# Performance work log

Measured on AMD Instinct MI355X. Metric: run time of the kernel, lower is better.

Reference implementation:

```python
import jax, jax.numpy as jnp
import numpy as np

B, S, E = 4, 4096, 128  # batch, seq_len, embedding_dim (quaternion groups)
D = 4 * E               # flattened feature dim fed to the Linear layers


def setup_inputs() -> dict:
    key = jax.random.key(0)
    ks = jax.random.split(key, 9)
    scale_w = 1.0 / np.sqrt(D).astype(np.float32)
    return {
        "query": jax.random.normal(ks[0], (B, S, E, 4), dtype=jnp.float32),
        "key": jax.random.normal(ks[1], (B, S, E, 4), dtype=jnp.float32),
        "value": jax.random.normal(ks[2], (B, S, E, 4), dtype=jnp.float32),
        "Wq": jax.random.normal(ks[3], (D, D), dtype=jnp.float32) * scale_w,
        "bq": jax.random.normal(ks[4], (D,), dtype=jnp.float32) * 0.01,
        "Wk": jax.random.normal(ks[5], (D, D), dtype=jnp.float32) * scale_w,
        "bk": jax.random.normal(ks[6], (D,), dtype=jnp.float32) * 0.01,
        "Wv": jax.random.normal(ks[7], (D, D), dtype=jnp.float32) * scale_w,
        "bv": jax.random.normal(ks[8], (D,), dtype=jnp.float32) * 0.01,
    }


def reference(query, key, value, Wq, bq, Wk, bk, Wv, bv):
    b, s = query.shape[0], query.shape[1]
    e = query.shape[2]  # embedding_dim
    # flatten quaternion dim: [B,S,E,4] -> [B,S,4E]
    q = query.reshape(b, s, -1)
    k = key.reshape(b, key.shape[1], -1)
    v = value.reshape(b, value.shape[1], -1)
    # torch nn.Linear: x @ W^T + bias
    Q = (q @ Wq.T + bq).reshape(b, s, -1, 4)
    K = (k @ Wk.T + bk).reshape(b, key.shape[1], -1, 4)
    V = (v @ Wv.T + bv).reshape(b, value.shape[1], -1, 4)
    # full QK^T over quaternion-grouped dims: [B,S,S]
    scores = jnp.einsum('bseq,bkeq->bsk', Q, K) / jnp.sqrt(jnp.float32(e))
    weights = jax.nn.softmax(scores, axis=-1)
    # faithful to the source: weights are summed over k and scale V at position s
    output = jnp.einsum('bsk,bseq->bseq', weights, V)
    return output, weights
```

## Files before the change

kernel.cpp:

```cpp
#include <hip/hip_runtime.h>
#include <cstdint>

typedef _Float16 h1;
typedef _Float16 h4 __attribute__((ext_vector_type(4)));
typedef _Float16 h8 __attribute__((ext_vector_type(8)));
typedef float    f4 __attribute__((ext_vector_type(4)));
typedef float    f32x4 __attribute__((ext_vector_type(4)));

#define NB 4
#define SL 4096
#define DD 512
#define MM (NB*SL)
#define SHIFT 12.0f

__global__ __launch_bounds__(256) void convert_all(
    const float* __restrict__ Xq, const float* __restrict__ Xk, const float* __restrict__ Xv,
    const float* __restrict__ Wq, const float* __restrict__ Wk, const float* __restrict__ Wv,
    h1* __restrict__ Xh, h1* __restrict__ Wh)
{
    const int xper = MM*DD/4;
    const int wper = DD*DD/4;
    const int xtot = 3*xper;
    int i = blockIdx.x * 256 + threadIdx.x;
    const float* src;
    h1* dst;
    int j;
    if (i < xtot) {
        int mat = i / xper; j = i - mat*xper;
        src = (mat==0) ? Xq : (mat==1 ? Xk : Xv);
        dst = Xh + (size_t)mat*MM*DD;
    } else {
        int t = i - xtot;
        if (t >= 3*wper) return;
        int mat = t / wper; j = t - mat*wper;
        src = (mat==0) ? Wq : (mat==1 ? Wk : Wv);
        dst = Wh + (size_t)mat*DD*DD;
    }
    f4 v = ((const f4*)src)[j];
    h4 hv;
    hv[0]=(h1)v[0]; hv[1]=(h1)v[1]; hv[2]=(h1)v[2]; hv[3]=(h1)v[3];
    ((h4*)dst)[j] = hv;
}

__device__ __forceinline__ void stage_tile(const h1* __restrict__ gbase,
                                           h1* lds, int w, int l)
{
    #pragma unroll
    for (int j = 0; j < 4; j++) {
        const int cc  = w*4 + j;
        const int row = cc*8 + (l >> 3);
        const int sc  = (l & 7) ^ (l >> 3);
        const h1* src = gbase + (size_t)row * DD + sc*8;
        void* dst = (char*)lds + cc*1024;
        __builtin_amdgcn_global_load_lds(
            (const __attribute__((address_space(1))) uint32_t*)src,
            (__attribute__((address_space(3))) uint32_t*)dst, 16, 0, 0);
    }
}

__device__ __forceinline__ h8 lds_frag(const h1* lds, int row, int lc)
{
    const int chunk = lc ^ (row & 7);
    return *(const h8*)(lds + row*64 + chunk*8);
}

__global__ __launch_bounds__(256) void proj_gemm(
    const h1* __restrict__ Xh, const h1* __restrict__ Wh,
    const float* __restrict__ bq, const float* __restrict__ bk, const float* __restrict__ bv,
    h1* __restrict__ Qh, h1* __restrict__ Kh, float* __restrict__ Vout)
{
    const int prj = blockIdx.z;
    const h1* __restrict__ X    = Xh + (size_t)prj * MM * DD;
    const h1* __restrict__ W    = Wh + (size_t)prj * DD * DD;
    const float* __restrict__ bias = (prj==0) ? bq : (prj==1 ? bk : bv);

    const int m0 = blockIdx.y * 128;
    const int n0 = blockIdx.x * 128;

    __shared__ h1 As[128*64];
    __shared__ h1 Bs[128*64];

    const int tid  = threadIdx.x;
    const int lane = tid & 63;
    const int wid  = tid >> 6;
    const int wm = wid >> 1, wn = wid & 1;
    const int g  = lane >> 4, c = lane & 15;

    f32x4 acc[4][4];
    #pragma unroll
    for (int i = 0; i < 4; i++)
        #pragma unroll
        for (int j = 0; j < 4; j++) acc[i][j] = (f32x4){0.f, 0.f, 0.f, 0.f};

    for (int k0 = 0; k0 < DD; k0 += 64) {
        __syncthreads();
        stage_tile(X + (size_t)m0 * DD + k0, As, wid, lane);
        stage_tile(W + (size_t)n0 * DD + k0, Bs, wid, lane);
        __syncthreads();
        #pragma unroll
        for (int kk = 0; kk < 2; kk++) {
            h8 af[4], bf[4];
            #pragma unroll
            for (int mf = 0; mf < 4; mf++) af[mf] = lds_frag(As, wm*64 + mf*16 + c, kk*4 + g);
            #pragma unroll
            for (int nf = 0; nf < 4; nf++) bf[nf] = lds_frag(Bs, wn*64 + nf*16 + c, kk*4 + g);
            #pragma unroll
            for (int mf = 0; mf < 4; mf++)
                #pragma unroll
                for (int nf = 0; nf < 4; nf++)
                    acc[mf][nf] = __builtin_amdgcn_mfma_f32_16x16x32_f16(af[mf], bf[nf], acc[mf][nf], 0, 0, 0);
        }
    }

    float bv4[4];
    #pragma unroll
    for (int nf = 0; nf < 4; nf++) bv4[nf] = bias[n0 + wn*64 + nf*16 + c];

    #pragma unroll
    for (int mf = 0; mf < 4; mf++) {
        #pragma unroll
        for (int i = 0; i < 4; i++) {
            const int row = m0 + wm*64 + mf*16 + g*4 + i;
            #pragma unroll
            for (int nf = 0; nf < 4; nf++) {
                const int col = n0 + wn*64 + nf*16 + c;
                float vv = acc[mf][nf][i] + bv4[nf];
                if (prj == 0)      Qh[(size_t)row*DD + col] = (h1)vv;
                else if (prj == 1) Kh[(size_t)row*DD + col] = (h1)vv;
                else               Vout[(size_t)row*DD + col] = vv;
            }
        }
    }
}

__device__ __forceinline__ void stage_slot32(const h1* __restrict__ gbase,
                                             char* ldsbase, int w, int l)
{
    #pragma unroll
    for (int j = 0; j < 2; j++) {
        const int lc  = j*512 + w*64 + l;
        const int row = lc >> 2;
        const int ch  = lc & 3;
        const int sc  = ch ^ ((row >> 1) & 3);
        const h1* src = gbase + (size_t)row * DD + sc*8;
        __builtin_amdgcn_global_load_lds(
            (const __attribute__((address_space(1))) uint32_t*)src,
            (__attribute__((address_space(3))) uint32_t*)(ldsbase + (size_t)(j*512 + w*64)*16),
            16, 0, 0);
    }
}

__device__ __forceinline__ h8 frag32(const h1* lds, int row, int g)
{
    const int ch = g ^ ((row >> 1) & 3);
    return *(const h8*)(lds + row*32 + ch*8);
}

__global__ __launch_bounds__(512) void scores_gemm_8ph(
    const h1* __restrict__ Qh, const h1* __restrict__ Kh,
    h1* __restrict__ Eh,
    float* __restrict__ partial)
{
    const int orig = blockIdx.x;
    const int swz  = (orig & 7) * 128 + (orig >> 3);
    const int b  = swz >> 8;
    const int t_ = swz & 255;
    const int ty = t_ >> 4;
    const int tx = t_ & 15;
    const int m0 = ty * 256;
    const int n0 = tx * 256;
    const h1* __restrict__ Qb = Qh + (size_t)b * SL * DD;
    const h1* __restrict__ Kb = Kh + (size_t)b * SL * DD;

    __shared__ h1 Albuf[4*256*32];
    __shared__ h1 Blbuf[4*256*32];
    const int SLOT_H = 256*32;
    const int SLOT_B = SLOT_H*2;

    const int tid  = threadIdx.x;
    const int lane = tid & 63;
    const int wid  = tid >> 6;
    const int wm = wid >> 2;
    const int wn = wid & 3;
    const int g  = lane >> 4, c = lane & 15;

    f32x4 acc[8][4];
    #pragma unroll
    for (int i = 0; i < 8; i++)
        #pragma unroll
        for (int j = 0; j < 4; j++) acc[i][j] = (f32x4){0.f, 0.f, 0.f, 0.f};

    #pragma unroll
    for (int kt = 0; kt < 3; ++kt) {
        stage_slot32(Qb + (size_t)m0*DD + kt*32, (char*)Albuf + kt*SLOT_B, wid, lane);
        stage_slot32(Kb + (size_t)n0*DD + kt*32, (char*)Blbuf + kt*SLOT_B, wid, lane);
    }
    asm volatile("s_waitcnt vmcnt(8)" ::: "memory");
    __builtin_amdgcn_s_barrier();

    for (int kt = 0; kt < 16; ++kt) {
        const int cur = kt & 3;
        const h1* Abase = Albuf + cur*SLOT_H;
        const h1* Bbase = Blbuf + cur*SLOT_H;

        h8 af[4], bf[4];
        #pragma unroll
        for (int fm = 0; fm < 4; fm++) af[fm] = frag32(Abase, wm*128 + fm*16 + c, g);
        #pragma unroll
        for (int fn = 0; fn < 4; fn++) bf[fn] = frag32(Bbase, wn*64 + fn*16 + c, g);

        if (kt <= 12) {
            const int nk = kt + 3, ns = nk & 3;
            stage_slot32(Qb + (size_t)m0*DD + nk*32, (char*)Albuf + ns*SLOT_B, wid, lane);
            stage_slot32(Kb + (size_t)n0*DD + nk*32, (char*)Blbuf + ns*SLOT_B, wid, lane);
        }

        __builtin_amdgcn_s_barrier();
        asm volatile("s_waitcnt lgkmcnt(0)" ::: "memory");
        __builtin_amdgcn_sched_barrier(0);
        __builtin_amdgcn_s_setprio(1);
        #pragma unroll
        for (int fm = 0; fm < 4; fm++)
            #pragma unroll
            for (int fn = 0; fn < 4; fn++)
                acc[fm][fn] = __builtin_amdgcn_mfma_f32_16x16x32_f16(af[fm], bf[fn], acc[fm][fn], 0, 0, 0);
        __builtin_amdgcn_s_setprio(0);
        __builtin_amdgcn_s_barrier();

        #pragma unroll
        for (int fm = 0; fm < 4; fm++) af[fm] = frag32(Abase, wm*128 + 64 + fm*16 + c, g);

        __builtin_amdgcn_s_barrier();
        asm volatile("s_waitcnt lgkmcnt(0)" ::: "memory");
        __builtin_amdgcn_sched_barrier(0);
        __builtin_amdgcn_s_setprio(1);
        #pragma unroll
        for (int fm = 0; fm < 4; fm++)
            #pragma unroll
            for (int fn = 0; fn < 4; fn++)
                acc[4+fm][fn] = __builtin_amdgcn_mfma_f32_16x16x32_f16(af[fm], bf[fn], acc[4+fm][fn], 0, 0, 0);
        __builtin_amdgcn_s_setprio(0);

        if (kt <= 12)      { asm volatile("s_waitcnt vmcnt(8)" ::: "memory"); }
        else if (kt == 13) { asm volatile("s_waitcnt vmcnt(4)" ::: "memory"); }
        else if (kt == 14) { asm volatile("s_waitcnt vmcnt(0)" ::: "memory"); }
        __builtin_amdgcn_s_barrier();
    }

    const float inv_scale = 0.08838834764831845f;
    #pragma unroll
    for (int mf = 0; mf < 8; mf++) {
        #pragma unroll
        for (int i = 0; i < 4; i++) {
            const int row = m0 + wm*128 + mf*16 + g*4 + i;
            h1* erow = Eh + ((size_t)b * SL + row) * SL;
            float rsum = 0.f;
            #pragma unroll
            for (int nf = 0; nf < 4; nf++) {
                const int col = n0 + wn*64 + nf*16 + c;
                float e = __expf(fmaf(acc[mf][nf][i], inv_scale, -SHIFT));
                erow[col] = (h1)e;
                rsum += e;
            }
            #pragma unroll
            for (int off = 1; off < 16; off <<= 1) rsum += __shfl_xor(rsum, off);
            if (c == 0)
                partial[((size_t)b * SL + row) * 64 + tx * 4 + wn] = rsum;
        }
    }
}

__global__ __launch_bounds__(256) void rowsum_inv(
    const float* __restrict__ partial, float* __restrict__ invrow)
{
    int row = blockIdx.x * 256 + threadIdx.x;
    const f4* p = (const f4*)(partial + (size_t)row * 64);
    float s = 0.f;
    #pragma unroll
    for (int i = 0; i < 16; i++) { f4 v = p[i]; s += v[0] + v[1] + v[2] + v[3]; }
    invrow[row] = 1.0f / s;
}

__global__ __launch_bounds__(256) void normalize_k(
    const h1* __restrict__ Eh, const float* __restrict__ invrow,
    float* __restrict__ Wout)
{
    const size_t total8 = (size_t)NB * SL * SL / 8;
    size_t i = (size_t)blockIdx.x * blockDim.x + threadIdx.x;
    const size_t stride = (size_t)gridDim.x * blockDim.x;
    for (; i < total8; i += stride) {
        const int row = (int)(i >> 9);
        h8 v = ((const h8*)Eh)[i];
        const float s = invrow[row];
        f4 o0, o1;
        #pragma unroll
        for (int j = 0; j < 4; j++) { o0[j] = (float)v[j] * s; o1[j] = (float)v[4+j] * s; }
        ((f4*)Wout)[i*2]   = o0;
        ((f4*)Wout)[i*2+1] = o1;
    }
}

extern "C" void kernel_launch(void* const* d_in, const int* in_sizes, int n_in,
                              void* d_out, int out_size, void* d_ws, size_t ws_size,
                              hipStream_t stream)
{
    const float* q  = (const float*)d_in[0];
    const float* k  = (const float*)d_in[1];
    const float* v  = (const float*)d_in[2];
    const float* Wq = (const float*)d_in[3];
    const float* bq = (const float*)d_in[4];
    const float* Wk = (const float*)d_in[5];
    const float* bk = (const float*)d_in[6];
    const float* Wv = (const float*)d_in[7];
    const float* bv = (const float*)d_in[8];

    float* out  = (float*)d_out;
    float* Vout = out;
    float* Wout = out + (size_t)MM * DD;

    char* ws = (char*)d_ws;
    h1* Xh = (h1*)ws;
    h1* Wh = (h1*)(ws + (size_t)3*MM*DD*2);
    h1* Qh = (h1*)((char*)Wh + (size_t)3*DD*DD*2);
    h1* Kh = (h1*)((char*)Qh + (size_t)MM*DD*2);
    float* partial = (float*)((char*)Kh + (size_t)MM*DD*2);
    float* invrow  = (float*)((char*)partial + (size_t)MM*64*4);
    h1* Eh = (h1*)((char*)invrow + (size_t)MM*4);

    const int conv_chunks = (3*MM*DD + 3*DD*DD) / 4;
    convert_all<<<(conv_chunks + 255)/256, 256, 0, stream>>>(q, k, v, Wq, Wk, Wv, Xh, Wh);
    proj_gemm<<<dim3(4, 128, 3), 256, 0, stream>>>(Xh, Wh, bq, bk, bv, Qh, Kh, Vout);
    scores_gemm_8ph<<<1024, 512, 0, stream>>>(Qh, Kh, Eh, partial);
    rowsum_inv<<<MM / 256, 256, 0, stream>>>(partial, invrow);
    normalize_k<<<2048, 256, 0, stream>>>(Eh, invrow, Wout);
}
```

Before: 285.3 us.

## Fuse all stages into one persistent cooperative kernel with grid syncs

Replaces the five separate launches (convert, projection GEMM, scores GEMM, row-sum inverse, normalize) with a single cooperative kernel of 256 blocks of 512 threads. Stages are separated by grid.sync, and blocks loop over tiles: the projection uses narrower 128x128 tiles split across 8 waves, and each block computes four 256x256 score tiles in turn. The aim is to remove launch gaps and inter-kernel tails. In exchange, occupancy is capped at one large block per CU, there are four grid-wide barriers, and the projection tiling is changed.

```diff
diff --git a/kernel.cpp b/kernel.cpp
--- a/kernel.cpp
+++ b/kernel.cpp
@@ -1,5 +1,8 @@
 #include <hip/hip_runtime.h>
+#include <hip/hip_cooperative_groups.h>
 #include <cstdint>
+
+namespace cg = cooperative_groups;
 
 typedef _Float16 h1;
 typedef _Float16 h4 __attribute__((ext_vector_type(4)));
@@ -12,49 +15,26 @@
 #define DD 512
 #define MM (NB*SL)
 #define SHIFT 12.0f
-
-__global__ __launch_bounds__(256) void convert_all(
-    const float* __restrict__ Xq, const float* __restrict__ Xk, const float* __restrict__ Xv,
-    const float* __restrict__ Wq, const float* __restrict__ Wk, const float* __restrict__ Wv,
-    h1* __restrict__ Xh, h1* __restrict__ Wh)
-{
-    const int xper = MM*DD/4;
-    const int wper = DD*DD/4;
-    const int xtot = 3*xper;
-    int i = blockIdx.x * 256 + threadIdx.x;
-    const float* src;
-    h1* dst;
-    int j;
-    if (i < xtot) {
-        int mat = i / xper; j = i - mat*xper;
-        src = (mat==0) ? Xq : (mat==1 ? Xk : Xv);
-        dst = Xh + (size_t)mat*MM*DD;
-    } else {
-        int t = i - xtot;
-        if (t >= 3*wper) return;
-        int mat = t / wper; j = t - mat*wper;
-        src = (mat==0) ? Wq : (mat==1 ? Wk : Wv);
-        dst = Wh + (size_t)mat*DD*DD;
-    }
-    f4 v = ((const f4*)src)[j];
-    h4 hv;
-    hv[0]=(h1)v[0]; hv[1]=(h1)v[1]; hv[2]=(h1)v[2]; hv[3]=(h1)v[3];
-    ((h4*)dst)[j] = hv;
-}
-
-__device__ __forceinline__ void stage_tile(const h1* __restrict__ gbase,
-                                           h1* lds, int w, int l)
+#define NTHREADS 131072
+
+struct Params {
+    const float *Xq, *Xk, *Xv, *Wq, *Wk, *Wv, *bq, *bk, *bv;
+    h1 *Xh, *Wh, *Qh, *Kh, *Eh;
+    float *partial, *invrow, *Vout, *Wout;
+};
+
+__device__ __forceinline__ void stage_half(const h1* __restrict__ gbase,
+                                           char* ldsbase, int w, int l)
 {
     #pragma unroll
-    for (int j = 0; j < 4; j++) {
-        const int cc  = w*4 + j;
+    for (int j = 0; j < 2; j++) {
+        const int cc  = w*2 + j;
         const int row = cc*8 + (l >> 3);
         const int sc  = (l & 7) ^ (l >> 3);
         const h1* src = gbase + (size_t)row * DD + sc*8;
-        void* dst = (char*)lds + cc*1024;
         __builtin_amdgcn_global_load_lds(
             (const __attribute__((address_space(1))) uint32_t*)src,
-            (__attribute__((address_space(3))) uint32_t*)dst, 16, 0, 0);
+            (__attribute__((address_space(3))) uint32_t*)(ldsbase + cc*1024), 16, 0, 0);
     }
 }
 
@@ -62,75 +42,6 @@
 {
     const int chunk = lc ^ (row & 7);
     return *(const h8*)(lds + row*64 + chunk*8);
-}
-
-__global__ __launch_bounds__(256) void proj_gemm(
-    const h1* __restrict__ Xh, const h1* __restrict__ Wh,
-    const float* __restrict__ bq, const float* __restrict__ bk, const float* __restrict__ bv,
-    h1* __restrict__ Qh, h1* __restrict__ Kh, float* __restrict__ Vout)
-{
-    const int prj = blockIdx.z;
-    const h1* __restrict__ X    = Xh + (size_t)prj * MM * DD;
-    const h1* __restrict__ W    = Wh + (size_t)prj * DD * DD;
-    const float* __restrict__ bias = (prj==0) ? bq : (prj==1 ? bk : bv);
-
-    const int m0 = blockIdx.y * 128;
-    const int n0 = blockIdx.x * 128;
-
-    __shared__ h1 As[128*64];
-    __shared__ h1 Bs[128*64];
-
-    const int tid  = threadIdx.x;
-    const int lane = tid & 63;
-    const int wid  = tid >> 6;
-    const int wm = wid >> 1, wn = wid & 1;
-    const int g  = lane >> 4, c = lane & 15;
-
-    f32x4 acc[4][4];
-    #pragma unroll
-    for (int i = 0; i < 4; i++)
-        #pragma unroll
-        for (int j = 0; j < 4; j++) acc[i][j] = (f32x4){0.f, 0.f, 0.f, 0.f};
-
-    for (int k0 = 0; k0 < DD; k0 += 64) {
-        __syncthreads();
-        stage_tile(X + (size_t)m0 * DD + k0, As, wid, lane);
-        stage_tile(W + (size_t)n0 * DD + k0, Bs, wid, lane);
-        __syncthreads();
-        #pragma unroll
-        for (int kk = 0; kk < 2; kk++) {
-            h8 af[4], bf[4];
-            #pragma unroll
-            for (int mf = 0; mf < 4; mf++) af[mf] = lds_frag(As, wm*64 + mf*16 + c, kk*4 + g);
-            #pragma unroll
-            for (int nf = 0; nf < 4; nf++) bf[nf] = lds_frag(Bs, wn*64 + nf*16 + c, kk*4 + g);
-            #pragma unroll
-            for (int mf = 0; mf < 4; mf++)
-                #pragma unroll
-                for (int nf = 0; nf < 4; nf++)
-                    acc[mf][nf] = __builtin_amdgcn_mfma_f32_16x16x32_f16(af[mf], bf[nf], acc[mf][nf], 0, 0, 0);
-        }
-    }
-
-    float bv4[4];
-    #pragma unroll
-    for (int nf = 0; nf < 4; nf++) bv4[nf] = bias[n0 + wn*64 + nf*16 + c];
-
-    #pragma unroll
-    for (int mf = 0; mf < 4; mf++) {
-        #pragma unroll
-        for (int i = 0; i < 4; i++) {
-            const int row = m0 + wm*64 + mf*16 + g*4 + i;
-            #pragma unroll
-            for (int nf = 0; nf < 4; nf++) {
-                const int col = n0 + wn*64 + nf*16 + c;
-                float vv = acc[mf][nf][i] + bv4[nf];
-                if (prj == 0)      Qh[(size_t)row*DD + col] = (h1)vv;
-                else if (prj == 1) Kh[(size_t)row*DD + col] = (h1)vv;
-                else               Vout[(size_t)row*DD + col] = vv;
-            }
-        }
-    }
 }
 
 __device__ __forceinline__ void stage_slot32(const h1* __restrict__ gbase,
@@ -156,147 +67,239 @@
     return *(const h8*)(lds + row*32 + ch*8);
 }
 
-__global__ __launch_bounds__(512) void scores_gemm_8ph(
-    const h1* __restrict__ Qh, const h1* __restrict__ Kh,
-    h1* __restrict__ Eh,
-    float* __restrict__ partial)
-{
-    const int orig = blockIdx.x;
-    const int swz  = (orig & 7) * 128 + (orig >> 3);
-    const int b  = swz >> 8;
-    const int t_ = swz & 255;
-    const int ty = t_ >> 4;
-    const int tx = t_ & 15;
-    const int m0 = ty * 256;
-    const int n0 = tx * 256;
-    const h1* __restrict__ Qb = Qh + (size_t)b * SL * DD;
-    const h1* __restrict__ Kb = Kh + (size_t)b * SL * DD;
-
-    __shared__ h1 Albuf[4*256*32];
-    __shared__ h1 Blbuf[4*256*32];
-    const int SLOT_H = 256*32;
-    const int SLOT_B = SLOT_H*2;
+__global__ __launch_bounds__(512) void mega(Params p)
+{
+    cg::grid_group grid = cg::this_grid();
+    __shared__ char smem[131072];
 
     const int tid  = threadIdx.x;
+    const int bid  = blockIdx.x;
+    const int gtid = bid * 512 + tid;
     const int lane = tid & 63;
     const int wid  = tid >> 6;
-    const int wm = wid >> 2;
-    const int wn = wid & 3;
-    const int g  = lane >> 4, c = lane & 15;
-
-    f32x4 acc[8][4];
-    #pragma unroll
-    for (int i = 0; i < 8; i++)
+    const int g    = lane >> 4, c = lane & 15;
+
+    {
+        const int xper = MM*DD/4;
+        const int wper = DD*DD/4;
+        const int xtot = 3*xper;
+        const int tot  = xtot + 3*wper;
+        for (int i = gtid; i < tot; i += NTHREADS) {
+            const float* src;
+            h1* dst;
+            int j;
+            if (i < xtot) {
+                int mat = i / xper; j = i - mat*xper;
+                src = (mat==0) ? p.Xq : (mat==1 ? p.Xk : p.Xv);
+                dst = p.Xh + (size_t)mat*MM*DD;
+            } else {
+                int t = i - xtot;
+                int mat = t / wper; j = t - mat*wper;
+                src = (mat==0) ? p.Wq : (mat==1 ? p.Wk : p.Wv);
+                dst = p.Wh + (size_t)mat*DD*DD;
+            }
+            f4 v = ((const f4*)src)[j];
+            h4 hv;
+            hv[0]=(h1)v[0]; hv[1]=(h1)v[1]; hv[2]=(h1)v[2]; hv[3]=(h1)v[3];
+            ((h4*)dst)[j] = hv;
+        }
+    }
+    grid.sync();
+
+    {
+        h1* As = (h1*)smem;
+        h1* Bs = (h1*)(smem + 16384);
+        const int wm = wid >> 2;
+        const int wn = wid & 3;
+
+        for (int tile = bid; tile < 1536; tile += 256) {
+            const int prj = tile >> 9;
+            const int rem = tile & 511;
+            const int m0  = (rem >> 2) * 128;
+            const int n0  = (rem & 3) * 128;
+            const h1* X = p.Xh + (size_t)prj * MM * DD;
+            const h1* W = p.Wh + (size_t)prj * DD * DD;
+            const float* bias = (prj==0) ? p.bq : (prj==1 ? p.bk : p.bv);
+
+            f32x4 acc[4][2];
+            #pragma unroll
+            for (int i = 0; i < 4; i++)
+                #pragma unroll
+                for (int j = 0; j < 2; j++) acc[i][j] = (f32x4){0.f,0.f,0.f,0.f};
+
+            for (int k0 = 0; k0 < DD; k0 += 64) {
+                __syncthreads();
+                stage_half(X + (size_t)m0 * DD + k0, (char*)As, wid, lane);
+                stage_half(W + (size_t)n0 * DD + k0, (char*)Bs, wid, lane);
+                __syncthreads();
+                #pragma unroll
+                for (int kk = 0; kk < 2; kk++) {
+                    h8 af[4], bf[2];
+                    #pragma unroll
+                    for (int mf = 0; mf < 4; mf++) af[mf] = lds_frag(As, wm*64 + mf*16 + c, kk*4 + g);
+                    #pragma unroll
+                    for (int nf = 0; nf < 2; nf++) bf[nf] = lds_frag(Bs, wn*32 + nf*16 + c, kk*4 + g);
+                    #pragma unroll
+                    for (int mf = 0; mf < 4; mf++)
+                        #pragma unroll
+                        for (int nf = 0; nf < 2; nf++)
+                            acc[mf][nf] = __builtin_amdgcn_mfma_f32_16x16x32_f16(af[mf], bf[nf], acc[mf][nf], 0, 0, 0);
+                }
+            }
+
+            float bv2[2];
+            #pragma unroll
+            for (int nf = 0; nf < 2; nf++) bv2[nf] = bias[n0 + wn*32 + nf*16 + c];
+
+            #pragma unroll
+            for (int mf = 0; mf < 4; mf++) {
+                #pragma unroll
+                for (int i = 0; i < 4; i++) {
+                    const int row = m0 + wm*64 + mf*16 + g*4 + i;
+                    #pragma unroll
+                    for (int nf = 0; nf < 2; nf++) {
+                        const int col = n0 + wn*32 + nf*16 + c;
+                        float vv = acc[mf][nf][i] + bv2[nf];
+                        if (prj == 0)      p.Qh[(size_t)row*DD + col] = (h1)vv;
+                        else if (prj == 1) p.Kh[(size_t)row*DD + col] = (h1)vv;
+                        else               p.Vout[(size_t)row*DD + col] = vv;
+                    }
+                }
+            }
+            __syncthreads();
+        }
+    }
+    grid.sync();
+
+    {
+        h1* Albuf = (h1*)smem;
+        h1* Blbuf = (h1*)(smem + 65536);
+        const int SLOT_H = 256*32;
+        const int SLOT_B = SLOT_H*2;
+        const int wm = wid >> 2;
+        const int wn = wid & 3;
+        const float inv_scale = 0.08838834764831845f;
+
+        #pragma unroll 1
+        for (int tt = 0; tt < 4; tt++) {
+            const int t_ = bid*4 + tt;
+            const int b  = t_ >> 8;
+            const int ty = (t_ >> 4) & 15;
+            const int tx = t_ & 15;
+            const int m0 = ty * 256;
+            const int n0 = tx * 256;
+            const h1* __restrict__ Qb = p.Qh + (size_t)b * SL * DD;
+            const h1* __restrict__ Kb = p.Kh + (size_t)b * SL * DD;
+
+            f32x4 acc[8][4];
+            #pragma unroll
+            for (int i = 0; i < 8; i++)
+                #pragma unroll
+                for (int j = 0; j < 4; j++) acc[i][j] = (f32x4){0.f,0.f,0.f,0.f};
+
+            __syncthreads();
+            #pragma unroll
+            for (int kt = 0; kt < 3; ++kt) {
+                stage_slot32(Qb + (size_t)m0*DD + kt*32, (char*)Albuf + kt*SLOT_B, wid, lane);
+                stage_slot32(Kb + (size_t)n0*DD + kt*32, (char*)Blbuf + kt*SLOT_B, wid, lane);
+            }
+            asm volatile("s_waitcnt vmcnt(8)" ::: "memory");
+            __builtin_amdgcn_s_barrier();
+
+            for (int kt = 0; kt < 16; ++kt) {
+                const int cur = kt & 3;
+                const h1* Abase = Albuf + cur*SLOT_H;
+                const h1* Bbase = Blbuf + cur*SLOT_H;
+
+                h8 af[4], bf[4];
+                #pragma unroll
+                for (int fm = 0; fm < 4; fm++) af[fm] = frag32(Abase, wm*128 + fm*16 + c, g);
+                #pragma unroll
+                for (int fn = 0; fn < 4; fn++) bf[fn] = frag32(Bbase, wn*64 + fn*16 + c, g);
+
+                if (kt <= 12) {
+                    const int nk = kt + 3, ns = nk & 3;
+                    stage_slot32(Qb + (size_t)m0*DD + nk*32, (char*)Albuf + ns*SLOT_B, wid, lane);
+                    stage_slot32(Kb + (size_t)n0*DD + nk*32, (char*)Blbuf + ns*SLOT_B, wid, lane);
+                }
+
+                __builtin_amdgcn_s_barrier();
+                asm volatile("s_waitcnt lgkmcnt(0)" ::: "memory");
+                __builtin_amdgcn_sched_barrier(0);
+                __builtin_amdgcn_s_setprio(1);
+                #pragma unroll
+                for (int fm = 0; fm < 4; fm++)
+                    #pragma unroll
+                    for (int fn = 0; fn < 4; fn++)
+                        acc[fm][fn] = __builtin_amdgcn_mfma_f32_16x16x32_f16(af[fm], bf[fn], acc[fm][fn], 0, 0, 0);
+                __builtin_amdgcn_s_setprio(0);
+                __builtin_amdgcn_s_barrier();
+
+                #pragma unroll
+                for (int fm = 0; fm < 4; fm++) af[fm] = frag32(Abase, wm*128 + 64 + fm*16 + c, g);
+
+                __builtin_amdgcn_s_barrier();
+                asm volatile("s_waitcnt lgkmcnt(0)" ::: "memory");
+                __builtin_amdgcn_sched_barrier(0);
+                __builtin_amdgcn_s_setprio(1);
+                #pragma unroll
+                for (int fm = 0; fm < 4; fm++)
+                    #pragma unroll
+                    for (int fn = 0; fn < 4; fn++)
+                        acc[4+fm][fn] = __builtin_amdgcn_mfma_f32_16x16x32_f16(af[fm], bf[fn], acc[4+fm][fn], 0, 0, 0);
+                __builtin_amdgcn_s_setprio(0);
+
+                if (kt <= 12)      { asm volatile("s_waitcnt vmcnt(8)" ::: "memory"); }
+                else if (kt == 13) { asm volatile("s_waitcnt vmcnt(4)" ::: "memory"); }
+                else if (kt == 14) { asm volatile("s_waitcnt vmcnt(0)" ::: "memory"); }
+                __builtin_amdgcn_s_barrier();
+            }
+
+            #pragma unroll
+            for (int mf = 0; mf < 8; mf++) {
+                #pragma unroll
+                for (int i = 0; i < 4; i++) {
+                    const int row = m0 + wm*128 + mf*16 + g*4 + i;
+                    h1* erow = p.Eh + ((size_t)b * SL + row) * SL;
+                    float rsum = 0.f;
+                    #pragma unroll
+                    for (int nf = 0; nf < 4; nf++) {
+                        const int col = n0 + wn*64 + nf*16 + c;
+                        float e = __expf(fmaf(acc[mf][nf][i], inv_scale, -SHIFT));
+                        erow[col] = (h1)e;
+                        rsum += e;
+                    }
+                    #pragma unroll
+                    for (int off = 1; off < 16; off <<= 1) rsum += __shfl_xor(rsum, off);
+                    if (c == 0)
+                        p.partial[((size_t)b * SL + row) * 64 + tx * 4 + wn] = rsum;
+                }
+            }
+        }
+    }
+    grid.sync();
+
+    if (gtid < MM) {
+        const f4* pp = (const f4*)(p.partial + (size_t)gtid * 64);
+        float s = 0.f;
         #pragma unroll
-        for (int j = 0; j < 4; j++) acc[i][j] = (f32x4){0.f, 0.f, 0.f, 0.f};
-
-    #pragma unroll
-    for (int kt = 0; kt < 3; ++kt) {
-        stage_slot32(Qb + (size_t)m0*DD + kt*32, (char*)Albuf + kt*SLOT_B, wid, lane);
-        stage_slot32(Kb + (size_t)n0*DD + kt*32, (char*)Blbuf + kt*SLOT_B, wid, lane);
-    }
-    asm volatile("s_waitcnt vmcnt(8)" ::: "memory");
-    __builtin_amdgcn_s_barrier();
-
-    for (int kt = 0; kt < 16; ++kt) {
-        const int cur = kt & 3;
-        const h1* Abase = Albuf + cur*SLOT_H;
-        const h1* Bbase = Blbuf + cur*SLOT_H;
-
-        h8 af[4], bf[4];
-        #pragma unroll
-        for (int fm = 0; fm < 4; fm++) af[fm] = frag32(Abase, wm*128 + fm*16 + c, g);
-        #pragma unroll
-        for (int fn = 0; fn < 4; fn++) bf[fn] = frag32(Bbase, wn*64 + fn*16 + c, g);
-
-        if (kt <= 12) {
-            const int nk = kt + 3, ns = nk & 3;
-            stage_slot32(Qb + (size_t)m0*DD + nk*32, (char*)Albuf + ns*SLOT_B, wid, lane);
-            stage_slot32(Kb + (size_t)n0*DD + nk*32, (char*)Blbuf + ns*SLOT_B, wid, lane);
+        for (int i = 0; i < 16; i++) { f4 v = pp[i]; s += v[0] + v[1] + v[2] + v[3]; }
+        p.invrow[gtid] = 1.0f / s;
+    }
+    grid.sync();
+
+    {
+        const size_t total8 = (size_t)NB * SL * SL / 8;
+        for (size_t i = gtid; i < total8; i += NTHREADS) {
+            const int row = (int)(i >> 9);
+            h8 v = ((const h8*)p.Eh)[i];
+            const float s = p.invrow[row];
+            f4 o0, o1;
+            #pragma unroll
+            for (int j = 0; j < 4; j++) { o0[j] = (float)v[j] * s; o1[j] = (float)v[4+j] * s; }
+            ((f4*)p.Wout)[i*2]   = o0;
+            ((f4*)p.Wout)[i*2+1] = o1;
         }
-
-        __builtin_amdgcn_s_barrier();
-        asm volatile("s_waitcnt lgkmcnt(0)" ::: "memory");
-        __builtin_amdgcn_sched_barrier(0);
-        __builtin_amdgcn_s_setprio(1);
-        #pragma unroll
-        for (int fm = 0; fm < 4; fm++)
-            #pragma unroll
-            for (int fn = 0; fn < 4; fn++)
-                acc[fm][fn] = __builtin_amdgcn_mfma_f32_16x16x32_f16(af[fm], bf[fn], acc[fm][fn], 0, 0, 0);
-        __builtin_amdgcn_s_setprio(0);
-        __builtin_amdgcn_s_barrier();
-
-        #pragma unroll
-        for (int fm = 0; fm < 4; fm++) af[fm] = frag32(Abase, wm*128 + 64 + fm*16 + c, g);
-
-        __builtin_amdgcn_s_barrier();
-        asm volatile("s_waitcnt lgkmcnt(0)" ::: "memory");
-        __builtin_amdgcn_sched_barrier(0);
-        __builtin_amdgcn_s_setprio(1);
-        #pragma unroll
-        for (int fm = 0; fm < 4; fm++)
-            #pragma unroll
-            for (int fn = 0; fn < 4; fn++)
-                acc[4+fm][fn] = __builtin_amdgcn_mfma_f32_16x16x32_f16(af[fm], bf[fn], acc[4+fm][fn], 0, 0, 0);
-        __builtin_amdgcn_s_setprio(0);
-
-        if (kt <= 12)      { asm volatile("s_waitcnt vmcnt(8)" ::: "memory"); }
-        else if (kt == 13) { asm volatile("s_waitcnt vmcnt(4)" ::: "memory"); }
-        else if (kt == 14) { asm volatile("s_waitcnt vmcnt(0)" ::: "memory"); }
-        __builtin_amdgcn_s_barrier();
-    }
-
-    const float inv_scale = 0.08838834764831845f;
-    #pragma unroll
-    for (int mf = 0; mf < 8; mf++) {
-        #pragma unroll
-        for (int i = 0; i < 4; i++) {
-            const int row = m0 + wm*128 + mf*16 + g*4 + i;
-            h1* erow = Eh + ((size_t)b * SL + row) * SL;
-            float rsum = 0.f;
-            #pragma unroll
-            for (int nf = 0; nf < 4; nf++) {
-                const int col = n0 + wn*64 + nf*16 + c;
-                float e = __expf(fmaf(acc[mf][nf][i], inv_scale, -SHIFT));
-                erow[col] = (h1)e;
-                rsum += e;
-            }
-            #pragma unroll
-            for (int off = 1; off < 16; off <<= 1) rsum += __shfl_xor(rsum, off);
-            if (c == 0)
-                partial[((size_t)b * SL + row) * 64 + tx * 4 + wn] = rsum;
-        }
-    }
-}
-
-__global__ __launch_bounds__(256) void rowsum_inv(
-    const float* __restrict__ partial, float* __restrict__ invrow)
-{
-    int row = blockIdx.x * 256 + threadIdx.x;
-    const f4* p = (const f4*)(partial + (size_t)row * 64);
-    float s = 0.f;
-    #pragma unroll
-    for (int i = 0; i < 16; i++) { f4 v = p[i]; s += v[0] + v[1] + v[2] + v[3]; }
-    invrow[row] = 1.0f / s;
-}
-
-__global__ __launch_bounds__(256) void normalize_k(
-    const h1* __restrict__ Eh, const float* __restrict__ invrow,
-    float* __restrict__ Wout)
-{
-    const size_t total8 = (size_t)NB * SL * SL / 8;
-    size_t i = (size_t)blockIdx.x * blockDim.x + threadIdx.x;
-    const size_t stride = (size_t)gridDim.x * blockDim.x;
-    for (; i < total8; i += stride) {
-        const int row = (int)(i >> 9);
-        h8 v = ((const h8*)Eh)[i];
-        const float s = invrow[row];
-        f4 o0, o1;
-        #pragma unroll
-        for (int j = 0; j < 4; j++) { o0[j] = (float)v[j] * s; o1[j] = (float)v[4+j] * s; }
-        ((f4*)Wout)[i*2]   = o0;
-        ((f4*)Wout)[i*2+1] = o1;
     }
 }
 
@@ -304,33 +307,31 @@
                               void* d_out, int out_size, void* d_ws, size_t ws_size,
                               hipStream_t stream)
 {
-    const float* q  = (const float*)d_in[0];
-    const float* k  = (const float*)d_in[1];
-    const float* v  = (const float*)d_in[2];
-    const float* Wq = (const float*)d_in[3];
-    const float* bq = (const float*)d_in[4];
-    const float* Wk = (const float*)d_in[5];
-    const float* bk = (const float*)d_in[6];
-    const float* Wv = (const float*)d_in[7];
-    const float* bv = (const float*)d_in[8];
-
     float* out  = (float*)d_out;
-    float* Vout = out;
-    float* Wout = out + (size_t)MM * DD;
-
     char* ws = (char*)d_ws;
-    h1* Xh = (h1*)ws;
-    h1* Wh = (h1*)(ws + (size_t)3*MM*DD*2);
-    h1* Qh = (h1*)((char*)Wh + (size_t)3*DD*DD*2);
-    h1* Kh = (h1*)((char*)Qh + (size_t)MM*DD*2);
-    float* partial = (float*)((char*)Kh + (size_t)MM*DD*2);
-    float* invrow  = (float*)((char*)partial + (size_t)MM*64*4);
-    h1* Eh = (h1*)((char*)invrow + (size_t)MM*4);
-
-    const int conv_chunks = (3*MM*DD + 3*DD*DD) / 4;
-    convert_all<<<(conv_chunks + 255)/256, 256, 0, stream>>>(q, k, v, Wq, Wk, Wv, Xh, Wh);
-    proj_gemm<<<dim3(4, 128, 3), 256, 0, stream>>>(Xh, Wh, bq, bk, bv, Qh, Kh, Vout);
-    scores_gemm_8ph<<<1024, 512, 0, stream>>>(Qh, Kh, Eh, partial);
-    rowsum_inv<<<MM / 256, 256, 0, stream>>>(partial, invrow);
-    normalize_k<<<2048, 256, 0, stream>>>(Eh, invrow, Wout);
-}
+
+    Params hp;
+    hp.Xq = (const float*)d_in[0];
+    hp.Xk = (const float*)d_in[1];
+    hp.Xv = (const float*)d_in[2];
+    hp.Wq = (const float*)d_in[3];
+    hp.bq = (const float*)d_in[4];
+    hp.Wk = (const float*)d_in[5];
+    hp.bk = (const float*)d_in[6];
+    hp.Wv = (const float*)d_in[7];
+    hp.bv = (const float*)d_in[8];
+
+    hp.Vout = out;
+    hp.Wout = out + (size_t)MM * DD;
+
+    hp.Xh = (h1*)ws;
+    hp.Wh = (h1*)(ws + (size_t)3*MM*DD*2);
+    hp.Qh = (h1*)((char*)hp.Wh + (size_t)3*DD*DD*2);
+    hp.Kh = (h1*)((char*)hp.Qh + (size_t)MM*DD*2);
+    hp.partial = (float*)((char*)hp.Kh + (size_t)MM*DD*2);
+    hp.invrow  = (float*)((char*)hp.partial + (size_t)MM*64*4);
+    hp.Eh = (h1*)((char*)hp.invrow + (size_t)MM*4);
+
+    void* args[] = { &hp };
+    hipLaunchCooperativeKernel((const void*)mega, dim3(256), dim3(512), args, 0, stream);
+}
```

After: 478.9 us. 67.8% more time.

## Stage fp16 epilogue stores through LDS and fuse rowsum into normalize

Applied to the files above, without the earlier changes.

Half-precision outputs of the projection and scores GEMMs are first written to a per-wave LDS slab, then flushed to global memory as 16-byte row-contiguous stores. Before, each lane wrote scattered 2-byte elements. The separate rowsum_inv and normalize_k kernels are merged into one per-row kernel that reduces the 64 partial sums and normalizes the row. This aims to cut uncoalesced write traffic and one kernel launch plus the invrow round trip. The cost is extra LDS traffic, wave barriers in the epilogue, and reuse of the staging buffers after the main loop.

```diff
diff --git a/kernel.cpp b/kernel.cpp
--- a/kernel.cpp
+++ b/kernel.cpp
@@ -64,75 +64,6 @@
     return *(const h8*)(lds + row*64 + chunk*8);
 }
 
-__global__ __launch_bounds__(256) void proj_gemm(
-    const h1* __restrict__ Xh, const h1* __restrict__ Wh,
-    const float* __restrict__ bq, const float* __restrict__ bk, const float* __restrict__ bv,
-    h1* __restrict__ Qh, h1* __restrict__ Kh, float* __restrict__ Vout)
-{
-    const int prj = blockIdx.z;
-    const h1* __restrict__ X    = Xh + (size_t)prj * MM * DD;
-    const h1* __restrict__ W    = Wh + (size_t)prj * DD * DD;
-    const float* __restrict__ bias = (prj==0) ? bq : (prj==1 ? bk : bv);
-
-    const int m0 = blockIdx.y * 128;
-    const int n0 = blockIdx.x * 128;
-
-    __shared__ h1 As[128*64];
-    __shared__ h1 Bs[128*64];
-
-    const int tid  = threadIdx.x;
-    const int lane = tid & 63;
-    const int wid  = tid >> 6;
-    const int wm = wid >> 1, wn = wid & 1;
-    const int g  = lane >> 4, c = lane & 15;
-
-    f32x4 acc[4][4];
-    #pragma unroll
-    for (int i = 0; i < 4; i++)
-        #pragma unroll
-        for (int j = 0; j < 4; j++) acc[i][j] = (f32x4){0.f, 0.f, 0.f, 0.f};
-
-    for (int k0 = 0; k0 < DD; k0 += 64) {
-        __syncthreads();
-        stage_tile(X + (size_t)m0 * DD + k0, As, wid, lane);
-        stage_tile(W + (size_t)n0 * DD + k0, Bs, wid, lane);
-        __syncthreads();
-        #pragma unroll
-        for (int kk = 0; kk < 2; kk++) {
-            h8 af[4], bf[4];
-            #pragma unroll
-            for (int mf = 0; mf < 4; mf++) af[mf] = lds_frag(As, wm*64 + mf*16 + c, kk*4 + g);
-            #pragma unroll
-            for (int nf = 0; nf < 4; nf++) bf[nf] = lds_frag(Bs, wn*64 + nf*16 + c, kk*4 + g);
-            #pragma unroll
-            for (int mf = 0; mf < 4; mf++)
-                #pragma unroll
-                for (int nf = 0; nf < 4; nf++)
-                    acc[mf][nf] = __builtin_amdgcn_mfma_f32_16x16x32_f16(af[mf], bf[nf], acc[mf][nf], 0, 0, 0);
-        }
-    }
-
-    float bv4[4];
-    #pragma unroll
-    for (int nf = 0; nf < 4; nf++) bv4[nf] = bias[n0 + wn*64 + nf*16 + c];
-
-    #pragma unroll
-    for (int mf = 0; mf < 4; mf++) {
-        #pragma unroll
-        for (int i = 0; i < 4; i++) {
-            const int row = m0 + wm*64 + mf*16 + g*4 + i;
-            #pragma unroll
-            for (int nf = 0; nf < 4; nf++) {
-                const int col = n0 + wn*64 + nf*16 + c;
-                float vv = acc[mf][nf][i] + bv4[nf];
-                if (prj == 0)      Qh[(size_t)row*DD + col] = (h1)vv;
-                else if (prj == 1) Kh[(size_t)row*DD + col] = (h1)vv;
-                else               Vout[(size_t)row*DD + col] = vv;
-            }
-        }
-    }
-}
-
 __device__ __forceinline__ void stage_slot32(const h1* __restrict__ gbase,
                                              char* ldsbase, int w, int l)
 {
@@ -156,6 +87,112 @@
     return *(const h8*)(lds + row*32 + ch*8);
 }
 
+__device__ __forceinline__ void slab_write16(h1* slab, const float (&vals)[4][4], int g, int c)
+{
+    #pragma unroll
+    for (int i = 0; i < 4; i++)
+        #pragma unroll
+        for (int nf = 0; nf < 4; nf++)
+            slab[(g*4+i)*72 + nf*16 + c] = (h1)vals[i][nf];
+}
+
+__device__ __forceinline__ void slab_flush(const h1* slab, int lane, h1* gdst0, int grow)
+{
+    __builtin_amdgcn_wave_barrier();
+    asm volatile("s_waitcnt lgkmcnt(0)" ::: "memory");
+    const int rl = lane >> 3, ch = lane & 7;
+    h8 v0 = *(const h8*)(slab + rl*72 + ch*8);
+    h8 v1 = *(const h8*)(slab + (8+rl)*72 + ch*8);
+    *(h8*)(gdst0 + (size_t)rl*grow + ch*8)     = v0;
+    *(h8*)(gdst0 + (size_t)(8+rl)*grow + ch*8) = v1;
+    __builtin_amdgcn_wave_barrier();
+}
+
+__global__ __launch_bounds__(256) void proj_gemm(
+    const h1* __restrict__ Xh, const h1* __restrict__ Wh,
+    const float* __restrict__ bq, const float* __restrict__ bk, const float* __restrict__ bv,
+    h1* __restrict__ Qh, h1* __restrict__ Kh, float* __restrict__ Vout)
+{
+    const int prj = blockIdx.z;
+    const h1* __restrict__ X    = Xh + (size_t)prj * MM * DD;
+    const h1* __restrict__ W    = Wh + (size_t)prj * DD * DD;
+    const float* __restrict__ bias = (prj==0) ? bq : (prj==1 ? bk : bv);
+
+    const int m0 = blockIdx.y * 128;
+    const int n0 = blockIdx.x * 128;
+
+    __shared__ h1 As[128*64];
+    __shared__ h1 Bs[128*64];
+
+    const int tid  = threadIdx.x;
+    const int lane = tid & 63;
+    const int wid  = tid >> 6;
+    const int wm = wid >> 1, wn = wid & 1;
+    const int g  = lane >> 4, c = lane & 15;
+
+    f32x4 acc[4][4];
+    #pragma unroll
+    for (int i = 0; i < 4; i++)
+        #pragma unroll
+        for (int j = 0; j < 4; j++) acc[i][j] = (f32x4){0.f, 0.f, 0.f, 0.f};
+
+    for (int k0 = 0; k0 < DD; k0 += 64) {
+        __syncthreads();
+        stage_tile(X + (size_t)m0 * DD + k0, As, wid, lane);
+        stage_tile(W + (size_t)n0 * DD + k0, Bs, wid, lane);
+        __syncthreads();
+        #pragma unroll
+        for (int kk = 0; kk < 2; kk++) {
+            h8 af[4], bf[4];
+            #pragma unroll
+            for (int mf = 0; mf < 4; mf++) af[mf] = lds_frag(As, wm*64 + mf*16 + c, kk*4 + g);
+            #pragma unroll
+            for (int nf = 0; nf < 4; nf++) bf[nf] = lds_frag(Bs, wn*64 + nf*16 + c, kk*4 + g);
+            #pragma unroll
+            for (int mf = 0; mf < 4; mf++)
+                #pragma unroll
+                for (int nf = 0; nf < 4; nf++)
+                    acc[mf][nf] = __builtin_amdgcn_mfma_f32_16x16x32_f16(af[mf], bf[nf], acc[mf][nf], 0, 0, 0);
+        }
+    }
+
+    float bv4[4];
+    #pragma unroll
+    for (int nf = 0; nf < 4; nf++) bv4[nf] = bias[n0 + wn*64 + nf*16 + c];
+
+    __syncthreads();
+
+    if (prj < 2) {
+        h1* dstbase = (prj == 0) ? Qh : Kh;
+        h1* slab = As + wid*1152;
+        #pragma unroll
+        for (int mf = 0; mf < 4; mf++) {
+            float vals[4][4];
+            #pragma unroll
+            for (int i = 0; i < 4; i++)
+                #pragma unroll
+                for (int nf = 0; nf < 4; nf++)
+                    vals[i][nf] = acc[mf][nf][i] + bv4[nf];
+            slab_write16(slab, vals, g, c);
+            slab_flush(slab, lane,
+                       dstbase + (size_t)(m0 + wm*64 + mf*16)*DD + n0 + wn*64, DD);
+        }
+    } else {
+        #pragma unroll
+        for (int mf = 0; mf < 4; mf++) {
+            #pragma unroll
+            for (int i = 0; i < 4; i++) {
+                const int row = m0 + wm*64 + mf*16 + g*4 + i;
+                #pragma unroll
+                for (int nf = 0; nf < 4; nf++) {
+                    const int col = n0 + wn*64 + nf*16 + c;
+                    Vout[(size_t)row*DD + col] = acc[mf][nf][i] + bv4[nf];
+                }
+            }
+        }
+    }
+}
+
 __global__ __launch_bounds__(512) void scores_gemm_8ph(
     const h1* __restrict__ Qh, const h1* __restrict__ Kh,
     h1* __restrict__ Eh,
@@ -248,18 +285,18 @@
     }
 
     const float inv_scale = 0.08838834764831845f;
+    h1* slab = Albuf + wid*1152;
     #pragma unroll
     for (int mf = 0; mf < 8; mf++) {
+        float vals[4][4];
         #pragma unroll
         for (int i = 0; i < 4; i++) {
             const int row = m0 + wm*128 + mf*16 + g*4 + i;
-            h1* erow = Eh + ((size_t)b * SL + row) * SL;
             float rsum = 0.f;
             #pragma unroll
             for (int nf = 0; nf < 4; nf++) {
-                const int col = n0 + wn*64 + nf*16 + c;
                 float e = __expf(fmaf(acc[mf][nf][i], inv_scale, -SHIFT));
-                erow[col] = (h1)e;
+                vals[i][nf] = e;
                 rsum += e;
             }
             #pragma unroll
@@ -267,36 +304,38 @@
             if (c == 0)
                 partial[((size_t)b * SL + row) * 64 + tx * 4 + wn] = rsum;
         }
-    }
-}
-
-__global__ __launch_bounds__(256) void rowsum_inv(
-    const float* __restrict__ partial, float* __restrict__ invrow)
-{
-    int row = blockIdx.x * 256 + threadIdx.x;
-    const f4* p = (const f4*)(partial + (size_t)row * 64);
-    float s = 0.f;
-    #pragma unroll
-    for (int i = 0; i < 16; i++) { f4 v = p[i]; s += v[0] + v[1] + v[2] + v[3]; }
-    invrow[row] = 1.0f / s;
-}
-
-__global__ __launch_bounds__(256) void normalize_k(
-    const h1* __restrict__ Eh, const float* __restrict__ invrow,
+        slab_write16(slab, vals, g, c);
+        slab_flush(slab, lane,
+                   Eh + ((size_t)b * SL + m0 + wm*128 + mf*16) * SL + n0 + wn*64, SL);
+    }
+}
+
+__global__ __launch_bounds__(256) void rownorm(
+    const float* __restrict__ partial, const h1* __restrict__ Eh,
     float* __restrict__ Wout)
 {
-    const size_t total8 = (size_t)NB * SL * SL / 8;
-    size_t i = (size_t)blockIdx.x * blockDim.x + threadIdx.x;
-    const size_t stride = (size_t)gridDim.x * blockDim.x;
-    for (; i < total8; i += stride) {
-        const int row = (int)(i >> 9);
-        h8 v = ((const h8*)Eh)[i];
-        const float s = invrow[row];
+    const int row = blockIdx.x;
+    const int tid = threadIdx.x;
+    __shared__ float sinv;
+    if (tid < 64) {
+        float s = partial[(size_t)row * 64 + tid];
+        #pragma unroll
+        for (int off = 32; off > 0; off >>= 1) s += __shfl_xor(s, off);
+        if (tid == 0) sinv = 1.0f / s;
+    }
+    __syncthreads();
+    const float s = sinv;
+    const h8* er = (const h8*)(Eh + (size_t)row * SL);
+    f4* wr = (f4*)(Wout + (size_t)row * SL);
+    #pragma unroll
+    for (int jj = 0; jj < 2; jj++) {
+        const int j = tid + jj*256;
+        h8 v = er[j];
         f4 o0, o1;
         #pragma unroll
-        for (int j = 0; j < 4; j++) { o0[j] = (float)v[j] * s; o1[j] = (float)v[4+j] * s; }
-        ((f4*)Wout)[i*2]   = o0;
-        ((f4*)Wout)[i*2+1] = o1;
+        for (int x = 0; x < 4; x++) { o0[x] = (float)v[x] * s; o1[x] = (float)v[4+x] * s; }
+        wr[2*j]   = o0;
+        wr[2*j+1] = o1;
     }
 }
 
@@ -331,6 +370,5 @@
     convert_all<<<(conv_chunks + 255)/256, 256, 0, stream>>>(q, k, v, Wq, Wk, Wv, Xh, Wh);
     proj_gemm<<<dim3(4, 128, 3), 256, 0, stream>>>(Xh, Wh, bq, bk, bv, Qh, Kh, Vout);
     scores_gemm_8ph<<<1024, 512, 0, stream>>>(Qh, Kh, Eh, partial);
-    rowsum_inv<<<MM / 256, 256, 0, stream>>>(partial, invrow);
-    normalize_k<<<2048, 256, 0, stream>>>(Eh, invrow, Wout);
-}
+    rownorm<<<MM, 256, 0, stream>>>(partial, Eh, Wout);
+}
```

Result: faster. 264.9 us (median of 2 runs) (-7.2%).
